# Kernel tuning notes

Hardware: AMD Instinct MI355X
Metric: run time of the kernel (lower is better)

Reference implementation:

```python
import jax, jax.numpy as jnp
import numpy as np

B, T, D, H, E = 4, 2048, 1024, 2048, 8

def setup_inputs() -> dict:
    key = jax.random.key(0)
    ks = jax.random.split(key, 7)
    s_in = 1.0 / np.sqrt(D)
    s_hid = 1.0 / np.sqrt(H)
    return {
        "x": jax.random.normal(ks[0], (B, T, D), dtype=jnp.float32),
        "Wg": jax.random.uniform(ks[1], (D, E), jnp.float32, -s_in, s_in),
        "bg": jax.random.uniform(ks[2], (E,), jnp.float32, -s_in, s_in),
        "W1": jax.random.uniform(ks[3], (E, D, H), jnp.float32, -s_in, s_in),
        "b1": jax.random.uniform(ks[4], (E, H), jnp.float32, -s_in, s_in),
        "W2": jax.random.uniform(ks[5], (E, H, D), jnp.float32, -s_hid, s_hid),
        "b2": jax.random.uniform(ks[6], (E, D), jnp.float32, -s_hid, s_hid),
    }

def reference(x, Wg, bg, W1, b1, W2, b2):
    # gating: [B,T,E]
    gate = jax.nn.softmax(jnp.einsum('btd,de->bte', x, Wg) + bg, axis=-1)
    # all experts densely: hidden [B,T,E,H]
    h = jax.nn.relu(jnp.einsum('btd,edh->bteh', x, W1) + b1)
    # expert outputs [B,T,E,D]
    eo = jnp.einsum('bteh,ehd->bted', h, W2) + b2
    # softmax-weighted sum over experts -> [B,T,D]
    return jnp.einsum('bte,bted->btd', gate, eo)
```

## Files before the change

### kernel.cpp

```cpp
#include <hip/hip_runtime.h>
#include <hip/hip_bf16.h>
#include <stdint.h>


typedef __bf16 bf16_t;
typedef bf16_t bf16x8 __attribute__((ext_vector_type(8)));
typedef bf16_t bf16x4 __attribute__((ext_vector_type(4)));
typedef float  f32x4  __attribute__((ext_vector_type(4)));

#define Ddim 1024
#define Hdim 2048
#define Edim 8
#define Mdim 8192

__device__ __forceinline__ void async16(const void* g, const void* l) {
  __builtin_amdgcn_global_load_lds(
      (const __attribute__((address_space(1))) void*)(uintptr_t)g,
      (__attribute__((address_space(3))) void*)(uint32_t)(uintptr_t)l,
      16, 0, 0);
}

#define MFMA(a, b, c) __builtin_amdgcn_mfma_f32_16x16x32_bf16((a), (b), (c), 0, 0, 0)

#define WAIT_VM0() do {                                    \
    asm volatile("s_waitcnt vmcnt(0)" ::: "memory");       \
    __builtin_amdgcn_sched_barrier(0);                     \
  } while (0)

__global__ void gating_cvt_kernel(const float* __restrict__ x,
                                  const float* __restrict__ Wg,
                                  const float* __restrict__ bg,
                                  float* __restrict__ gate,
                                  bf16_t* __restrict__ xb) {
  const int lane = threadIdx.x & 63;
  const int wid  = threadIdx.x >> 6;
  const int t    = blockIdx.x * 4 + wid;
  const float* xr = x + (size_t)t * Ddim;
  bf16_t* xbr = xb + (size_t)t * Ddim;
  float acc[8] = {0.f,0.f,0.f,0.f,0.f,0.f,0.f,0.f};
  for (int i = lane; i < Ddim; i += 64) {
    float xv = xr[i];
    xbr[i] = (bf16_t)xv;
    f32x4 a = *(const f32x4*)(Wg + (size_t)i * 8);
    f32x4 b = *(const f32x4*)(Wg + (size_t)i * 8 + 4);
    acc[0] += xv * a[0]; acc[1] += xv * a[1];
    acc[2] += xv * a[2]; acc[3] += xv * a[3];
    acc[4] += xv * b[0]; acc[5] += xv * b[1];
    acc[6] += xv * b[2]; acc[7] += xv * b[3];
  }
  #pragma unroll
  for (int e = 0; e < 8; ++e) {
    #pragma unroll
    for (int off = 32; off; off >>= 1)
      acc[e] += __shfl_xor(acc[e], off, 64);
  }
  if (lane == 0) {
    float l[8], mx = -1e30f;
    #pragma unroll
    for (int e = 0; e < 8; ++e) { l[e] = acc[e] + bg[e]; mx = fmaxf(mx, l[e]); }
    float s = 0.f;
    #pragma unroll
    for (int e = 0; e < 8; ++e) { l[e] = __expf(l[e] - mx); s += l[e]; }
    float inv = 1.f / s;
    #pragma unroll
    for (int e = 0; e < 8; ++e) gate[(size_t)t * 8 + e] = l[e] * inv;
  }
}

__global__ void transpose_both(const float* __restrict__ W1s,
                               const float* __restrict__ W2s,
                               bf16_t* __restrict__ W1t,
                               bf16_t* __restrict__ W2t) {
  __shared__ bf16_t tile[32][33];
  const int G = gridDim.y >> 1;
  const int z = blockIdx.y;
  const float* src; bf16_t* dst; int C, bx, by;
  if (z < G) {
    src = W1s + (size_t)z * Ddim * Hdim;
    dst = W1t + (size_t)z * Ddim * Hdim;
    C = Hdim; bx = blockIdx.x & 63; by = blockIdx.x >> 6;
  } else {
    const int e = z - G;
    src = W2s + (size_t)e * Ddim * Hdim;
    dst = W2t + (size_t)e * Ddim * Hdim;
    C = Ddim; bx = blockIdx.x & 31; by = blockIdx.x >> 5;
  }
  const int R = (z < G) ? Ddim : Hdim;
  const int r0 = by * 32, c0 = bx * 32;
  const int tr = threadIdx.x >> 3;
  const int tc = (threadIdx.x & 7) * 4;
  f32x4 v = *(const f32x4*)(src + (size_t)(r0 + tr) * C + c0 + tc);
  tile[tr][tc+0] = (bf16_t)v[0]; tile[tr][tc+1] = (bf16_t)v[1];
  tile[tr][tc+2] = (bf16_t)v[2]; tile[tr][tc+3] = (bf16_t)v[3];
  __syncthreads();
  bf16x4 o;
  o[0] = tile[tc+0][tr]; o[1] = tile[tc+1][tr];
  o[2] = tile[tc+2][tr]; o[3] = tile[tc+3][tr];
  *(bf16x4*)(dst + (size_t)(c0 + tr) * R + r0 + tc) = o;
}

__launch_bounds__(512, 2)
__global__ void gemm1_kernel(const bf16_t* __restrict__ A,
                             const bf16_t* __restrict__ W1tAll,
                             const float*  __restrict__ gate,
                             const float*  __restrict__ b1,
                             bf16_t* __restrict__ hgAll,
                             int e0) {
  __shared__ alignas(16) bf16_t sA[2][256 * 64];
  __shared__ alignas(16) bf16_t sB[2][256 * 64];

  const int tid  = threadIdx.x;
  const int lane = tid & 63;
  const int wid  = tid >> 6;
  const int wm   = wid >> 2, wn = wid & 3;
  const int lrow = lane & 15, quad = lane >> 4;
  const int sb   = quad ^ (lrow & 7);

  const int z = blockIdx.z;
  const int e = e0 + z;
  const bf16_t* Bt = W1tAll + (size_t)z * Hdim * Ddim;
  bf16_t* hg = hgAll + (size_t)z * (size_t)Mdim * Hdim;
  const float* bias = b1 + (size_t)e * Hdim;

  const int bid = blockIdx.y * 8 + blockIdx.x;
  const int xcd = bid & 7, loc = bid >> 3;
  const int tileM = (xcd * 4 + (loc >> 3)) * 256;
  const int tileN = (loc & 7) * 256;

  const int trow = tid >> 3;
  const int tsw  = ((tid & 7) ^ (trow & 7)) << 4;
  const int ldst = tid << 4;
  const size_t SA = (size_t)64 * Ddim * 2;

  const char* a0 = (const char*)(A  + (size_t)(tileM + trow) * Ddim) + tsw;
  const char* b0 = (const char*)(Bt + (size_t)(tileN + trow) * Ddim) + tsw;
  char* curA = (char*)&sA[0][0]; char* nxtA = (char*)&sA[1][0];
  char* curB = (char*)&sB[0][0]; char* nxtB = (char*)&sB[1][0];

  async16(a0,          curA + 0 * 8192 + ldst);
  async16(a0 + SA,     curA + 1 * 8192 + ldst);
  async16(a0 + 2 * SA, curA + 2 * 8192 + ldst);
  async16(a0 + 3 * SA, curA + 3 * 8192 + ldst);
  async16(b0,          curB + 0 * 8192 + ldst);
  async16(b0 + SA,     curB + 1 * 8192 + ldst);
  async16(b0 + 2 * SA, curB + 2 * 8192 + ldst);
  async16(b0 + 3 * SA, curB + 3 * 8192 + ldst);
  a0 += 128; b0 += 128;
  WAIT_VM0();
  __builtin_amdgcn_s_barrier();

  f32x4 acc[8][4] = {};
  const int offA0 = (wm * 128 + lrow) * 128 + sb * 16;
  const int offA1 = (wm * 128 + lrow) * 128 + (sb ^ 4) * 16;
  const int offB0 = (wn * 64  + lrow) * 128 + sb * 16;
  const int offB1 = (wn * 64  + lrow) * 128 + (sb ^ 4) * 16;

  #pragma unroll 1
  for (int kk = 0; kk < Ddim / 64; ++kk) {
    const bool notlast = (kk + 1 < Ddim / 64);
    __builtin_amdgcn_sched_barrier(0);
    if (notlast) {
      async16(a0,          nxtA + 0 * 8192 + ldst);
      async16(a0 + SA,     nxtA + 1 * 8192 + ldst);
      async16(a0 + 2 * SA, nxtA + 2 * 8192 + ldst);
      async16(a0 + 3 * SA, nxtA + 3 * 8192 + ldst);
      async16(b0,          nxtB + 0 * 8192 + ldst);
      async16(b0 + SA,     nxtB + 1 * 8192 + ldst);
      async16(b0 + 2 * SA, nxtB + 2 * 8192 + ldst);
      async16(b0 + 3 * SA, nxtB + 3 * 8192 + ldst);
    }
    __builtin_amdgcn_sched_barrier(0);

    bf16x8 bfr[4][2];
    #pragma unroll
    for (int j = 0; j < 4; ++j) {
      bfr[j][0] = *(const bf16x8*)(curB + offB0 + j * 2048);
      bfr[j][1] = *(const bf16x8*)(curB + offB1 + j * 2048);
    }
    bf16x8 ca0 = *(const bf16x8*)(curA + offA0);
    bf16x8 ca1 = *(const bf16x8*)(curA + offA1);
    __builtin_amdgcn_s_setprio(1);
    #pragma unroll
    for (int i = 0; i < 8; ++i) {
      bf16x8 na0, na1;
      if (i < 7) {
        na0 = *(const bf16x8*)(curA + offA0 + (i + 1) * 2048);
        na1 = *(const bf16x8*)(curA + offA1 + (i + 1) * 2048);
      }
      #pragma unroll
      for (int j = 0; j < 4; ++j) {
        acc[i][j] = MFMA(ca0, bfr[j][0], acc[i][j]);
        acc[i][j] = MFMA(ca1, bfr[j][1], acc[i][j]);
      }
      if (i < 7) { ca0 = na0; ca1 = na1; }
    }
    __builtin_amdgcn_s_setprio(0);

    WAIT_VM0();
    __builtin_amdgcn_s_barrier();
    a0 += 128; b0 += 128;
    char* t;
    t = curA; curA = nxtA; nxtA = t;
    t = curB; curB = nxtB; nxtB = t;
  }

  const int col0 = tileN + wn * 64 + lrow;
  float bcol[4];
  #pragma unroll
  for (int j = 0; j < 4; ++j) bcol[j] = bias[col0 + j * 16];
  #pragma unroll
  for (int i = 0; i < 8; ++i) {
    #pragma unroll
    for (int r = 0; r < 4; ++r) {
      const int row = tileM + wm * 128 + i * 16 + quad * 4 + r;
      const float g = gate[(size_t)row * 8 + e];
      #pragma unroll
      for (int j = 0; j < 4; ++j) {
        float v = acc[i][j][r] + bcol[j];
        v = fmaxf(v, 0.f) * g;
        hg[(size_t)row * Hdim + col0 + j * 16] = (bf16_t)v;
      }
    }
  }
}

template <int G, bool FIRST>
__launch_bounds__(512, 2)
__global__ void gemm2_kernel(const bf16_t* __restrict__ hgAll,
                             const bf16_t* __restrict__ W2tAll,
                             const float*  __restrict__ gate,
                             const float*  __restrict__ b2,
                             float* __restrict__ out,
                             int e0) {
  __shared__ alignas(16) bf16_t sA[2][256 * 64];
  __shared__ alignas(16) bf16_t sB[2][128 * 64];

  const int tid  = threadIdx.x;
  const int lane = tid & 63;
  const int wid  = tid >> 6;
  const int wm   = wid >> 1, wn = wid & 1;
  const int lrow = lane & 15, quad = lane >> 4;
  const int sb   = quad ^ (lrow & 7);

  const int bid = blockIdx.y * 8 + blockIdx.x;
  const int xcd = bid & 7, loc = bid >> 3;
  const int tileM = (xcd * 4 + (loc >> 3)) * 256;
  const int tileN = (loc & 7) * 128;

  const int trow = tid >> 3;
  const int tsw  = ((tid & 7) ^ (trow & 7)) << 4;
  const int ldst = tid << 4;
  const size_t S = (size_t)64 * Hdim * 2;

  const char* a0 = (const char*)(hgAll  + (size_t)(tileM + trow) * Hdim) + tsw;
  const char* b0 = (const char*)(W2tAll + (size_t)(tileN + trow) * Hdim) + tsw;
  char* curA = (char*)&sA[0][0]; char* nxtA = (char*)&sA[1][0];
  char* curB = (char*)&sB[0][0]; char* nxtB = (char*)&sB[1][0];

  async16(a0,         curA + 0 * 8192 + ldst);
  async16(a0 + S,     curA + 1 * 8192 + ldst);
  async16(a0 + 2 * S, curA + 2 * 8192 + ldst);
  async16(a0 + 3 * S, curA + 3 * 8192 + ldst);
  async16(b0,         curB + 0 * 8192 + ldst);
  async16(b0 + S,     curB + 1 * 8192 + ldst);
  a0 += 128; b0 += 128;
  WAIT_VM0();
  __builtin_amdgcn_s_barrier();

  f32x4 acc[4][4] = {};
  const int offA0 = (wm * 64 + lrow) * 128 + sb * 16;
  const int offA1 = (wm * 64 + lrow) * 128 + (sb ^ 4) * 16;
  const int offB0 = (wn * 64 + lrow) * 128 + sb * 16;
  const int offB1 = (wn * 64 + lrow) * 128 + (sb ^ 4) * 16;

  const int NKT = G * (Hdim / 64);
  #pragma unroll 1
  for (int kk = 0; kk < NKT; ++kk) {
    const bool notlast = (kk + 1 < NKT);
    __builtin_amdgcn_sched_barrier(0);
    if (notlast && (((kk + 1) & 31) == 0)) {
      const int gn = (kk + 1) >> 5;
      a0 = (const char*)(hgAll  + (size_t)gn * Mdim * Hdim
                         + (size_t)(tileM + trow) * Hdim) + tsw;
      b0 = (const char*)(W2tAll + (size_t)gn * Ddim * Hdim
                         + (size_t)(tileN + trow) * Hdim) + tsw;
    }
    if (notlast) {
      async16(a0,         nxtA + 0 * 8192 + ldst);
      async16(a0 + S,     nxtA + 1 * 8192 + ldst);
      async16(a0 + 2 * S, nxtA + 2 * 8192 + ldst);
      async16(a0 + 3 * S, nxtA + 3 * 8192 + ldst);
      async16(b0,         nxtB + 0 * 8192 + ldst);
      async16(b0 + S,     nxtB + 1 * 8192 + ldst);
    }
    __builtin_amdgcn_sched_barrier(0);

    bf16x8 bfr[4][2];
    #pragma unroll
    for (int j = 0; j < 4; ++j) {
      bfr[j][0] = *(const bf16x8*)(curB + offB0 + j * 2048);
      bfr[j][1] = *(const bf16x8*)(curB + offB1 + j * 2048);
    }
    bf16x8 ca0 = *(const bf16x8*)(curA + offA0);
    bf16x8 ca1 = *(const bf16x8*)(curA + offA1);
    __builtin_amdgcn_s_setprio(1);
    #pragma unroll
    for (int i = 0; i < 4; ++i) {
      bf16x8 na0, na1;
      if (i < 3) {
        na0 = *(const bf16x8*)(curA + offA0 + (i + 1) * 2048);
        na1 = *(const bf16x8*)(curA + offA1 + (i + 1) * 2048);
      }
      #pragma unroll
      for (int j = 0; j < 4; ++j) {
        acc[i][j] = MFMA(ca0, bfr[j][0], acc[i][j]);
        acc[i][j] = MFMA(ca1, bfr[j][1], acc[i][j]);
      }
      if (i < 3) { ca0 = na0; ca1 = na1; }
    }
    __builtin_amdgcn_s_setprio(0);
    WAIT_VM0();
    __builtin_amdgcn_s_barrier();
    a0 += 128; b0 += 128;
    char* t;
    t = curA; curA = nxtA; nxtA = t;
    t = curB; curB = nxtB; nxtB = t;
  }

  const int col0 = tileN + wn * 64 + lrow;
  float b2c[4][G];
  #pragma unroll
  for (int j = 0; j < 4; ++j)
    #pragma unroll
    for (int g = 0; g < G; ++g)
      b2c[j][g] = b2[(size_t)(e0 + g) * Ddim + col0 + j * 16];

  #pragma unroll
  for (int i = 0; i < 4; ++i) {
    #pragma unroll
    for (int r = 0; r < 4; ++r) {
      const int row = tileM + wm * 64 + i * 16 + quad * 4 + r;
      const float* gr = gate + (size_t)row * 8 + e0;
      float gv[G];
      #pragma unroll
      for (int g = 0; g < G; ++g) gv[g] = gr[g];
      #pragma unroll
      for (int j = 0; j < 4; ++j) {
        float v = acc[i][j][r];
        #pragma unroll
        for (int g = 0; g < G; ++g) v += gv[g] * b2c[j][g];
        if (FIRST) out[(size_t)row * Ddim + col0 + j * 16] = v;
        else       out[(size_t)row * Ddim + col0 + j * 16] += v;
      }
    }
  }
}

extern "C" void kernel_launch(void* const* d_in, const int* in_sizes, int n_in,
                              void* d_out, int out_size, void* d_ws, size_t ws_size,
                              hipStream_t stream) {
  const float* x  = (const float*)d_in[0];
  const float* Wg = (const float*)d_in[1];
  const float* bg = (const float*)d_in[2];
  const float* W1 = (const float*)d_in[3];
  const float* b1 = (const float*)d_in[4];
  const float* W2 = (const float*)d_in[5];
  const float* b2 = (const float*)d_in[6];
  float* out = (float*)d_out;

  int G = 1;
  if      (ws_size >= (size_t)(17 + 40 * 8) << 20) G = 8;
  else if (ws_size >= (size_t)(17 + 40 * 4) << 20) G = 4;
  else if (ws_size >= (size_t)(17 + 40 * 2) << 20) G = 2;

  char* ws = (char*)d_ws;
  float*  gate = (float*)ws;
  bf16_t* xb   = (bf16_t*)(ws + (1u << 20));
  bf16_t* W1t  = (bf16_t*)(ws + (17u << 20));
  bf16_t* W2t  = (bf16_t*)(ws + ((size_t)(17 + 4 * G) << 20));
  bf16_t* hg   = (bf16_t*)(ws + ((size_t)(17 + 8 * G) << 20));

  gating_cvt_kernel<<<Mdim / 4, 256, 0, stream>>>(x, Wg, bg, gate, xb);

  const int nGroups = Edim / G;
  for (int gi = 0; gi < nGroups; ++gi) {
    const int e0 = gi * G;
    transpose_both<<<dim3(2048, 2 * G), 256, 0, stream>>>(
        W1 + (size_t)e0 * Ddim * Hdim, W2 + (size_t)e0 * Hdim * Ddim, W1t, W2t);

    gemm1_kernel<<<dim3(Hdim / 256, Mdim / 256, G), 512, 0, stream>>>(
        xb, W1t, gate, b1, hg, e0);

    const dim3 g2(Ddim / 128, Mdim / 256);
    const bool first = (gi == 0);
    if (G == 8)      gemm2_kernel<8, true ><<<g2, 512, 0, stream>>>(hg, W2t, gate, b2, out, e0);
    else if (G == 4) {
      if (first)     gemm2_kernel<4, true ><<<g2, 512, 0, stream>>>(hg, W2t, gate, b2, out, e0);
      else           gemm2_kernel<4, false><<<g2, 512, 0, stream>>>(hg, W2t, gate, b2, out, e0);
    } else if (G == 2) {
      if (first)     gemm2_kernel<2, true ><<<g2, 512, 0, stream>>>(hg, W2t, gate, b2, out, e0);
      else           gemm2_kernel<2, false><<<g2, 512, 0, stream>>>(hg, W2t, gate, b2, out, e0);
    } else {
      if (first)     gemm2_kernel<1, true ><<<g2, 512, 0, stream>>>(hg, W2t, gate, b2, out, e0);
      else           gemm2_kernel<1, false><<<g2, 512, 0, stream>>>(hg, W2t, gate, b2, out, e0);
    }
  }
}
```

Measured before the change: 695.6 us.

## Widen transpose tiles to 64 rows with 16-byte stores; preload all gemm2 A fragments

The weight transpose kernel now handles a 64x32 tile per block, with each thread loading two float4 rows and writing one 8-element bf16 vector instead of a 4-element one. The grid is halved to match. This is meant to cut the number of blocks and widen global stores. Separately, the gemm2 inner loop now loads all A fragments up front instead of double-buffering them per row, and one sched_barrier is removed. That gives the compiler freedom to schedule LDS reads, at the cost of more live registers.

```diff
diff --git a/kernel.cpp b/kernel.cpp
--- a/kernel.cpp
+++ b/kernel.cpp
@@ -71,32 +71,37 @@
                                const float* __restrict__ W2s,
                                bf16_t* __restrict__ W1t,
                                bf16_t* __restrict__ W2t) {
-  __shared__ bf16_t tile[32][33];
+  __shared__ bf16_t tile[64][33];
   const int G = gridDim.y >> 1;
   const int z = blockIdx.y;
-  const float* src; bf16_t* dst; int C, bx, by;
+  const float* src; bf16_t* dst; int R, C, br, bc;
   if (z < G) {
     src = W1s + (size_t)z * Ddim * Hdim;
     dst = W1t + (size_t)z * Ddim * Hdim;
-    C = Hdim; bx = blockIdx.x & 63; by = blockIdx.x >> 6;
+    R = Ddim; C = Hdim; bc = blockIdx.x & 63; br = blockIdx.x >> 6;
   } else {
     const int e = z - G;
     src = W2s + (size_t)e * Ddim * Hdim;
     dst = W2t + (size_t)e * Ddim * Hdim;
-    C = Ddim; bx = blockIdx.x & 31; by = blockIdx.x >> 5;
-  }
-  const int R = (z < G) ? Ddim : Hdim;
-  const int r0 = by * 32, c0 = bx * 32;
-  const int tr = threadIdx.x >> 3;
-  const int tc = (threadIdx.x & 7) * 4;
-  f32x4 v = *(const f32x4*)(src + (size_t)(r0 + tr) * C + c0 + tc);
-  tile[tr][tc+0] = (bf16_t)v[0]; tile[tr][tc+1] = (bf16_t)v[1];
-  tile[tr][tc+2] = (bf16_t)v[2]; tile[tr][tc+3] = (bf16_t)v[3];
+    R = Hdim; C = Ddim; bc = blockIdx.x & 31; br = blockIdx.x >> 5;
+  }
+  const int r0 = br * 64, c0 = bc * 32;
+  const int tid = threadIdx.x;
+  const int rr = tid >> 3, cc = (tid & 7) * 4;
+  #pragma unroll
+  for (int h = 0; h < 2; ++h) {
+    f32x4 v = *(const f32x4*)(src + (size_t)(r0 + rr + h * 32) * C + c0 + cc);
+    tile[rr + h * 32][cc + 0] = (bf16_t)v[0];
+    tile[rr + h * 32][cc + 1] = (bf16_t)v[1];
+    tile[rr + h * 32][cc + 2] = (bf16_t)v[2];
+    tile[rr + h * 32][cc + 3] = (bf16_t)v[3];
+  }
   __syncthreads();
-  bf16x4 o;
-  o[0] = tile[tc+0][tr]; o[1] = tile[tc+1][tr];
-  o[2] = tile[tc+2][tr]; o[3] = tile[tc+3][tr];
-  *(bf16x4*)(dst + (size_t)(c0 + tr) * R + r0 + tc) = o;
+  const int c = tid >> 3, ch = (tid & 7) * 8;
+  bf16x8 o;
+  #pragma unroll
+  for (int j = 0; j < 8; ++j) o[j] = tile[ch + j][c];
+  *(bf16x8*)(dst + (size_t)(c0 + c) * R + r0 + ch) = o;
 }
 
 __launch_bounds__(512, 2)
@@ -293,31 +298,25 @@
       async16(b0,         nxtB + 0 * 8192 + ldst);
       async16(b0 + S,     nxtB + 1 * 8192 + ldst);
     }
-    __builtin_amdgcn_sched_barrier(0);
-
-    bf16x8 bfr[4][2];
+    bf16x8 afr[4][2], bfr[4][2];
+    #pragma unroll
+    for (int i = 0; i < 4; ++i) {
+      afr[i][0] = *(const bf16x8*)(curA + offA0 + i * 2048);
+      afr[i][1] = *(const bf16x8*)(curA + offA1 + i * 2048);
+    }
     #pragma unroll
     for (int j = 0; j < 4; ++j) {
       bfr[j][0] = *(const bf16x8*)(curB + offB0 + j * 2048);
       bfr[j][1] = *(const bf16x8*)(curB + offB1 + j * 2048);
     }
-    bf16x8 ca0 = *(const bf16x8*)(curA + offA0);
-    bf16x8 ca1 = *(const bf16x8*)(curA + offA1);
     __builtin_amdgcn_s_setprio(1);
     #pragma unroll
-    for (int i = 0; i < 4; ++i) {
-      bf16x8 na0, na1;
-      if (i < 3) {
-        na0 = *(const bf16x8*)(curA + offA0 + (i + 1) * 2048);
-        na1 = *(const bf16x8*)(curA + offA1 + (i + 1) * 2048);
-      }
+    for (int i = 0; i < 4; ++i)
       #pragma unroll
       for (int j = 0; j < 4; ++j) {
-        acc[i][j] = MFMA(ca0, bfr[j][0], acc[i][j]);
-        acc[i][j] = MFMA(ca1, bfr[j][1], acc[i][j]);
+        acc[i][j] = MFMA(afr[i][0], bfr[j][0], acc[i][j]);
+        acc[i][j] = MFMA(afr[i][1], bfr[j][1], acc[i][j]);
       }
-      if (i < 3) { ca0 = na0; ca1 = na1; }
-    }
     __builtin_amdgcn_s_setprio(0);
     WAIT_VM0();
     __builtin_amdgcn_s_barrier();
@@ -385,7 +384,7 @@
   const int nGroups = Edim / G;
   for (int gi = 0; gi < nGroups; ++gi) {
     const int e0 = gi * G;
-    transpose_both<<<dim3(2048, 2 * G), 256, 0, stream>>>(
+    transpose_both<<<dim3(1024, 2 * G), 256, 0, stream>>>(
         W1 + (size_t)e0 * Ddim * Hdim, W2 + (size_t)e0 * Hdim * Ddim, W1t, W2t);
 
     gemm1_kernel<<<dim3(Hdim / 256, Mdim / 256, G), 512, 0, stream>>>(
```

Result: slower. 718.7 us (+3.3%).
